# Kernel tuning notes

Measured on AMD Instinct MI355X. Metric: run time of the kernel, lower is better.

Reference implementation:

```python
import jax, jax.numpy as jnp
import numpy as np


def setup_inputs() -> dict:
    key = jax.random.key(0)
    k1, k2, k3 = jax.random.split(key, 3)
    T, D, U = 32768, 1024, 1024
    x = jax.random.normal(k1, (1, T, D), dtype=jnp.float32)
    # scale weights down so gates don't saturate over long sequences
    kernel = jax.random.normal(k2, (D, 4 * U), dtype=jnp.float32) * 0.05
    recurrent_kernel = jax.random.normal(k3, (U, 4 * U), dtype=jnp.float32) * 0.05
    bias = jnp.zeros((4 * U,), dtype=jnp.float32)
    return {"x": x, "kernel": kernel, "recurrent_kernel": recurrent_kernel, "bias": bias}


def reference(x, kernel, recurrent_kernel, bias):
    # x: [1, T, D]; batch is fixed to 1 as in the original layer.
    U = recurrent_kernel.shape[0]
    xt = x[0]                              # [T, D]
    # Input contribution to gates can be precomputed (same math, hoisted out of the loop)
    zx = xt @ kernel + bias                # [T, 4U]

    def step(carry, z_x):
        h, c = carry                       # [U], [U]
        z = z_x + h @ recurrent_kernel     # [4U]
        zi, zf, zg, zo = jnp.split(z, 4)
        i = jax.nn.sigmoid(zi)
        f = jax.nn.sigmoid(zf)
        g = jnp.tanh(zg)
        o = jax.nn.sigmoid(zo)
        c = f * c + i * g
        h = o * jnp.tanh(c)
        return (h, c), h

    h0 = jnp.zeros((U,), dtype=x.dtype)
    c0 = jnp.zeros((U,), dtype=x.dtype)
    _, outputs = jax.lax.scan(step, (h0, c0), zx)   # [T, U]
    return outputs[None, :, :]                      # [1, T, U]
```

## Files before the change

### kernel.cpp

```cpp
#include <hip/hip_runtime.h>
#include <hip/hip_bf16.h>

#define T_STEPS 32768
#define DIM     1024
#define NGATE   4096
#define GWG     128
#define UPW     8

typedef __attribute__((ext_vector_type(8))) short  short8;
typedef __attribute__((ext_vector_type(4))) float  floatx4;

static __device__ __forceinline__ unsigned short f2bf(float f) {
    union { __hip_bfloat16 h; unsigned short u; } cv;
    cv.h = __float2bfloat16(f);
    return cv.u;
}
static __device__ __forceinline__ float fast_sigmoid(float x) {
    float e = __builtin_amdgcn_exp2f(x * -1.442695041f);
    return __builtin_amdgcn_rcpf(1.f + e);
}
static __device__ __forceinline__ float fast_tanh(float x) {
    float e = __builtin_amdgcn_exp2f(x * -2.885390082f);
    return __builtin_amdgcn_rcpf(1.f + e) * 2.f - 1.f;
}


__global__ void conv_x_kernel(const float* __restrict__ x,
                              unsigned short* __restrict__ xb, long n4) {
    long i = (long)blockIdx.x * blockDim.x + threadIdx.x;
    if (i >= n4) return;
    floatx4 v = ((const floatx4*)x)[i];
    unsigned long long p =  (unsigned long long)f2bf(v[0])
                         | ((unsigned long long)f2bf(v[1]) << 16)
                         | ((unsigned long long)f2bf(v[2]) << 32)
                         | ((unsigned long long)f2bf(v[3]) << 48);
    ((unsigned long long*)xb)[i] = p;
}

__global__ void conv_w_kernel(const float* __restrict__ kern,
                              unsigned short* __restrict__ wbt) {
    int idx = blockIdx.x * 256 + threadIdx.x;
    int kb  = idx >> 12;
    int c   = idx & 4095;
    int n = ((c & 1023) >> 3) * 32 + (c >> 10) * 8 + (c & 7);
    unsigned long long p = 0;
#pragma unroll
    for (int i = 0; i < 4; ++i) {
        float f = kern[(size_t)(kb * 4 + i) * NGATE + c];
        p |= (unsigned long long)f2bf(f) << (16 * i);
    }
    ((unsigned long long*)(wbt + (size_t)n * DIM))[kb] = p;
}

__global__ void init_kernel(long long* hbuf8, float* cst) {
    int t = threadIdx.x;
    for (int u = t; u < 1024; u += 256) {
        hbuf8[u]        = ((long long)(-2)) << 32;
        hbuf8[1024 + u] = ((long long)(-1)) << 32;
        cst[u] = 0.f;
    }
}


__global__ __launch_bounds__(256) void gemm_kernel(
        const unsigned short* __restrict__ xb,
        const unsigned short* __restrict__ wbt,
        float* __restrict__ zxf, int t0) {
    __shared__ unsigned short As[64 * 40];
    __shared__ unsigned short Bs[64 * 40];
    const int tid = threadIdx.x;
    const int w = tid >> 6, l = tid & 63;
    const int mBase = t0 + blockIdx.x * 64;
    const int nBase = blockIdx.y * 64;
    const int r  = tid >> 2;
    const int kc = (tid & 3) * 8;
    const int lm = l & 15, kq = l >> 4;

    floatx4 acc[4];
#pragma unroll
    for (int i = 0; i < 4; ++i) acc[i] = (floatx4){0.f, 0.f, 0.f, 0.f};

    for (int kt = 0; kt < DIM; kt += 32) {
        *(uint4*)&As[r * 40 + kc] = *(const uint4*)&xb [(size_t)(mBase + r) * DIM + kt + kc];
        *(uint4*)&Bs[r * 40 + kc] = *(const uint4*)&wbt[(size_t)(nBase + r) * DIM + kt + kc];
        __syncthreads();
        short8 a = *(const short8*)&As[(w * 16 + lm) * 40 + kq * 8];
#pragma unroll
        for (int i = 0; i < 4; ++i) {
            short8 b = *(const short8*)&Bs[(i * 16 + lm) * 40 + kq * 8];
            acc[i] = __builtin_amdgcn_mfma_f32_16x16x32_bf16(a, b, acc[i], 0, 0, 0);
        }
        __syncthreads();
    }
    const int rowq = (l >> 4) * 4;
#pragma unroll
    for (int i = 0; i < 4; ++i)
#pragma unroll
        for (int j = 0; j < 4; ++j) {
            int m = mBase + w * 16 + rowq + j;
            zxf[(size_t)(m - t0) * NGATE + nBase + i * 16 + lm] = acc[i][j];
        }
}


__global__ __launch_bounds__(256, 1) void scan_kernel(
        const float* __restrict__ zxf,
        const float* __restrict__ rker,
        const float* __restrict__ bias,
        float* __restrict__ out,
        long long* hbuf8, float* cst, int t0, int t1) {
    const int wg    = blockIdx.x;
    const int tid   = threadIdx.x;
    const int wave  = tid >> 6, lane = tid & 63;
    const int col32 = lane & 31;
    const int khalf = lane >> 5;
    const int kbase = (wave * 2 + khalf) * 128;
    const int gate  = col32 >> 3, uin = col32 & 7;
    const int c     = gate * 1024 + wg * UPW + uin;

    __shared__ float lds_h[1024];
    __shared__ float lds_part[2][3][32];

    float wr[128];
#pragma unroll
    for (int j = 0; j < 128; ++j)
        wr[j] = rker[(size_t)(kbase + j) * NGATE + c];

    float bias_v = bias[c];
    float cstate = 0.f;
    if (wave == 0 && lane < UPW) cstate = cst[wg * UPW + lane];

    for (int t = t0; t < t1; ++t) {
        const int par  = t & 1;
        const int rpar = (t + 1) & 1;
        const int etag = t - 1;

        float zxv = 0.f;
        if (wave == 0)
            zxv = zxf[(size_t)(t - t0) * NGATE + wg * 32 + col32];

        const long long* hb = hbuf8 + (size_t)rpar * 1024 + wave * 256 + lane * 4;
        int4 p0, p1;
        while (true) {
            asm volatile("global_load_dwordx4 %0, %2, off sc0 sc1\n\t"
                         "global_load_dwordx4 %1, %2, off offset:16 sc0 sc1\n\t"
                         "s_waitcnt vmcnt(0)"
                         : "=v"(p0), "=v"(p1) : "v"(hb) : "memory");
            bool ok = (p0.y == etag) && (p0.w == etag) &&
                      (p1.y == etag) && (p1.w == etag);
            if (__all(ok)) break;
        }

        floatx4 hv4;
        hv4[0] = __int_as_float(p0.x);
        hv4[1] = __int_as_float(p0.z);
        hv4[2] = __int_as_float(p1.x);
        hv4[3] = __int_as_float(p1.z);
        *(floatx4*)&lds_h[wave * 256 + lane * 4] = hv4;

        float z0 = 0.f, z1 = 0.f, z2 = 0.f, z3 = 0.f;
#pragma unroll
        for (int j = 0; j < 32; ++j) {
            floatx4 hv = *(const floatx4*)&lds_h[kbase + j * 4];
            z0 = fmaf(wr[4 * j + 0], hv[0], z0);
            z1 = fmaf(wr[4 * j + 1], hv[1], z1);
            z2 = fmaf(wr[4 * j + 2], hv[2], z2);
            z3 = fmaf(wr[4 * j + 3], hv[3], z3);
        }
        float z = (z0 + z1) + (z2 + z3);
        z += __shfl_down(z, 32);

        if (wave > 0 && lane < 32) lds_part[par][wave - 1][lane] = z;
        __syncthreads();

        if (wave == 0) {
            if (lane < 32) {
                z += lds_part[par][0][lane] + lds_part[par][1][lane] + lds_part[par][2][lane];
                z += bias_v + zxv;
            }
            int u = lane & 7;
            float g0 = __shfl(z,      u);
            float g1 = __shfl(z,  8 + u);
            float g2 = __shfl(z, 16 + u);
            float g3 = __shfl(z, 24 + u);
            if (lane < UPW) {
                float ig = fast_sigmoid(g0);
                float fg = fast_sigmoid(g1);
                float gg = fast_tanh(g2);
                float og = fast_sigmoid(g3);
                cstate = fg * cstate + ig * gg;
                float h = og * fast_tanh(cstate);
                out[(size_t)t * DIM + wg * UPW + lane] = h;
                int2 pr;
                pr.x = __float_as_int(h);
                pr.y = t;
                long long* dst = hbuf8 + (size_t)par * 1024 + wg * UPW + lane;
                asm volatile("global_store_dwordx2 %0, %1, off sc0 sc1"
                             :: "v"(dst), "v"(pr) : "memory");
            }
        }
    }
    if (wave == 0 && lane < UPW) cst[wg * UPW + lane] = cstate;
}


extern "C" void kernel_launch(void* const* d_in, const int* in_sizes, int n_in,
                              void* d_out, int out_size, void* d_ws, size_t ws_size,
                              hipStream_t stream) {
    const float* x    = (const float*)d_in[0];
    const float* kern = (const float*)d_in[1];
    const float* rker = (const float*)d_in[2];
    const float* bias = (const float*)d_in[3];
    float* out = (float*)d_out;

    char* ws = (char*)d_ws;
    size_t off = 0;
    auto alloc = [&](size_t bytes) {
        char* p = ws + off;
        off = (off + bytes + 255) & ~(size_t)255;
        return p;
    };
    unsigned short* wbt = (unsigned short*)alloc((size_t)NGATE * DIM * 2);
    unsigned short* xb  = (unsigned short*)alloc((size_t)T_STEPS * DIM * 2);
    long long* hbuf8 = (long long*)alloc(2 * 1024 * 8);
    float*     cst   = (float*)alloc(1024 * 4);

    size_t avail = ws_size > off ? ws_size - off : 0;
    size_t tcmax = avail / ((size_t)NGATE * 4);
    if (tcmax > T_STEPS) tcmax = T_STEPS;
    int TC = (int)(tcmax & ~(size_t)63);
    if (TC < 64) TC = 64;
    float* zxf = (float*)alloc((size_t)TC * NGATE * 4);

    hipLaunchKernelGGL(conv_w_kernel, dim3(4096), dim3(256), 0, stream, kern, wbt);
    hipLaunchKernelGGL(conv_x_kernel, dim3((T_STEPS * DIM / 4 + 255) / 256), dim3(256),
                       0, stream, x, xb, (long)(T_STEPS * DIM / 4));
    hipLaunchKernelGGL(init_kernel, dim3(1), dim3(256), 0, stream, hbuf8, cst);

    for (int t0 = 0; t0 < T_STEPS; t0 += TC) {
        int tc = (T_STEPS - t0 < TC) ? (T_STEPS - t0) : TC;
        hipLaunchKernelGGL(gemm_kernel, dim3(tc / 64, NGATE / 64), dim3(256),
                           0, stream, xb, wbt, zxf, t0);
        hipLaunchKernelGGL(scan_kernel, dim3(GWG), dim3(256),
                           0, stream, zxf, rker, bias, out, hbuf8, cst, t0, t0 + tc);
    }
}
```

Measured before the change: 68.21 ms.

## Replicate h broadcast buffers and remove intra-block reduction barrier in LSTM scan

Each of the 128 workgroups now polls one of 8 replicated copies of the hidden-state exchange buffer, and each producer writes its h values to all 8 copies, so polling traffic is spread across more memory lines. Work is remapped so each wave owns two units and reduces its dot product with cross-lane shuffles, which removes the LDS partial-sum stage and the wave-0 serial epilogue. The next step's zx value is prefetched. In exchange, each step issues eight times as many global stores, and the poll loop now uses per-element atomic loads instead of two wide loads.

```diff
diff --git a/kernel.cpp b/kernel.cpp
--- a/kernel.cpp
+++ b/kernel.cpp
@@ -6,6 +6,7 @@
 #define NGATE   4096
 #define GWG     128
 #define UPW     8
+#define NREP    8
 
 typedef __attribute__((ext_vector_type(8))) short  short8;
 typedef __attribute__((ext_vector_type(4))) float  floatx4;
@@ -55,8 +56,11 @@
 __global__ void init_kernel(long long* hbuf8, float* cst) {
     int t = threadIdx.x;
     for (int u = t; u < 1024; u += 256) {
-        hbuf8[u]        = ((long long)(-2)) << 32;
-        hbuf8[1024 + u] = ((long long)(-1)) << 32;
+#pragma unroll
+        for (int r = 0; r < NREP; ++r) {
+            hbuf8[(size_t)r * 2048 + u]        = ((long long)(-2)) << 32;
+            hbuf8[(size_t)r * 2048 + 1024 + u] = ((long long)(-1)) << 32;
+        }
         cst[u] = 0.f;
     }
 }
@@ -109,98 +113,104 @@
         const float* __restrict__ bias,
         float* __restrict__ out,
         long long* hbuf8, float* cst, int t0, int t1) {
-    const int wg    = blockIdx.x;
-    const int tid   = threadIdx.x;
-    const int wave  = tid >> 6, lane = tid & 63;
-    const int col32 = lane & 31;
-    const int khalf = lane >> 5;
-    const int kbase = (wave * 2 + khalf) * 128;
-    const int gate  = col32 >> 3, uin = col32 & 7;
-    const int c     = gate * 1024 + wg * UPW + uin;
-
-    __shared__ float lds_h[1024];
-    __shared__ float lds_part[2][3][32];
+    const int wg     = blockIdx.x;
+    const int tid    = threadIdx.x;
+    const int wave   = tid >> 6, lane = tid & 63;
+    const int kslice = lane >> 3;
+    const int idx8   = lane & 7;
+    const int g      = idx8 >> 1;
+    const int du     = idx8 & 1;
+    const int unit   = wg * UPW + 2 * wave + du;
+    const int c      = g * 1024 + unit;
+    const int zxcol  = wg * 32 + g * 8 + 2 * wave + du;
+    const int rep    = wg >> 4;
+
+    __shared__ float lds_h[2][8 * 132];
 
     float wr[128];
 #pragma unroll
     for (int j = 0; j < 128; ++j)
-        wr[j] = rker[(size_t)(kbase + j) * NGATE + c];
+        wr[j] = rker[(size_t)(kslice * 128 + j) * NGATE + c];
 
     float bias_v = bias[c];
     float cstate = 0.f;
-    if (wave == 0 && lane < UPW) cstate = cst[wg * UPW + lane];
+    if (lane < 2) cstate = cst[unit];
+
+    float zx_next = zxf[(size_t)0 * NGATE + zxcol];
+
+    const int stage_idx = (wave * 2 + (lane >> 5)) * 132 + (lane & 31) * 4;
 
     for (int t = t0; t < t1; ++t) {
         const int par  = t & 1;
         const int rpar = (t + 1) & 1;
         const int etag = t - 1;
-
-        float zxv = 0.f;
-        if (wave == 0)
-            zxv = zxf[(size_t)(t - t0) * NGATE + wg * 32 + col32];
-
-        const long long* hb = hbuf8 + (size_t)rpar * 1024 + wave * 256 + lane * 4;
-        int4 p0, p1;
-        while (true) {
-            asm volatile("global_load_dwordx4 %0, %2, off sc0 sc1\n\t"
-                         "global_load_dwordx4 %1, %2, off offset:16 sc0 sc1\n\t"
-                         "s_waitcnt vmcnt(0)"
-                         : "=v"(p0), "=v"(p1) : "v"(hb) : "memory");
-            bool ok = (p0.y == etag) && (p0.w == etag) &&
-                      (p1.y == etag) && (p1.w == etag);
-            if (__all(ok)) break;
-        }
-
-        floatx4 hv4;
-        hv4[0] = __int_as_float(p0.x);
-        hv4[1] = __int_as_float(p0.z);
-        hv4[2] = __int_as_float(p1.x);
-        hv4[3] = __int_as_float(p1.z);
-        *(floatx4*)&lds_h[wave * 256 + lane * 4] = hv4;
+        const float zxv = zx_next;
+
+        const long long* hb = hbuf8 + (size_t)rep * 2048 + (size_t)rpar * 1024
+                              + wave * 256 + lane * 4;
+        bool done = false;
+        do {
+            if (!done) {
+                long long q0 = __hip_atomic_load(hb + 0, __ATOMIC_RELAXED, __HIP_MEMORY_SCOPE_AGENT);
+                long long q1 = __hip_atomic_load(hb + 1, __ATOMIC_RELAXED, __HIP_MEMORY_SCOPE_AGENT);
+                long long q2 = __hip_atomic_load(hb + 2, __ATOMIC_RELAXED, __HIP_MEMORY_SCOPE_AGENT);
+                long long q3 = __hip_atomic_load(hb + 3, __ATOMIC_RELAXED, __HIP_MEMORY_SCOPE_AGENT);
+                if ((int)(q0 >> 32) == etag && (int)(q1 >> 32) == etag &&
+                    (int)(q2 >> 32) == etag && (int)(q3 >> 32) == etag) {
+                    floatx4 hv;
+                    hv[0] = __int_as_float((int)q0);
+                    hv[1] = __int_as_float((int)q1);
+                    hv[2] = __int_as_float((int)q2);
+                    hv[3] = __int_as_float((int)q3);
+                    *(floatx4*)&lds_h[rpar][stage_idx] = hv;
+                    done = true;
+                }
+            }
+        } while (!__all(done));
+        __syncthreads();
 
         float z0 = 0.f, z1 = 0.f, z2 = 0.f, z3 = 0.f;
+        const float* hp = &lds_h[rpar][kslice * 132];
 #pragma unroll
         for (int j = 0; j < 32; ++j) {
-            floatx4 hv = *(const floatx4*)&lds_h[kbase + j * 4];
+            floatx4 hv = *(const floatx4*)&hp[j * 4];
             z0 = fmaf(wr[4 * j + 0], hv[0], z0);
             z1 = fmaf(wr[4 * j + 1], hv[1], z1);
             z2 = fmaf(wr[4 * j + 2], hv[2], z2);
             z3 = fmaf(wr[4 * j + 3], hv[3], z3);
         }
         float z = (z0 + z1) + (z2 + z3);
-        z += __shfl_down(z, 32);
-
-        if (wave > 0 && lane < 32) lds_part[par][wave - 1][lane] = z;
-        __syncthreads();
-
-        if (wave == 0) {
-            if (lane < 32) {
-                z += lds_part[par][0][lane] + lds_part[par][1][lane] + lds_part[par][2][lane];
-                z += bias_v + zxv;
-            }
-            int u = lane & 7;
-            float g0 = __shfl(z,      u);
-            float g1 = __shfl(z,  8 + u);
-            float g2 = __shfl(z, 16 + u);
-            float g3 = __shfl(z, 24 + u);
-            if (lane < UPW) {
-                float ig = fast_sigmoid(g0);
-                float fg = fast_sigmoid(g1);
-                float gg = fast_tanh(g2);
-                float og = fast_sigmoid(g3);
-                cstate = fg * cstate + ig * gg;
-                float h = og * fast_tanh(cstate);
-                out[(size_t)t * DIM + wg * UPW + lane] = h;
-                int2 pr;
-                pr.x = __float_as_int(h);
-                pr.y = t;
-                long long* dst = hbuf8 + (size_t)par * 1024 + wg * UPW + lane;
+        z += __shfl_xor(z, 8);
+        z += __shfl_xor(z, 16);
+        z += __shfl_xor(z, 32);
+        z += bias_v + zxv;
+
+        int dl = lane & 1;
+        float gi = __shfl(z, dl);
+        float gf = __shfl(z, 2 + dl);
+        float gg = __shfl(z, 4 + dl);
+        float go = __shfl(z, 6 + dl);
+        if (lane < 2) {
+            float ig = fast_sigmoid(gi);
+            float fg = fast_sigmoid(gf);
+            float gv = fast_tanh(gg);
+            float og = fast_sigmoid(go);
+            cstate = fg * cstate + ig * gv;
+            float h = og * fast_tanh(cstate);
+            int2 pr;
+            pr.x = __float_as_int(h);
+            pr.y = t;
+            long long* dst = hbuf8 + (size_t)par * 1024 + unit;
+#pragma unroll
+            for (int r = 0; r < NREP; ++r)
                 asm volatile("global_store_dwordx2 %0, %1, off sc0 sc1"
-                             :: "v"(dst), "v"(pr) : "memory");
-            }
-        }
-    }
-    if (wave == 0 && lane < UPW) cst[wg * UPW + lane] = cstate;
+                             :: "v"(dst + (size_t)r * 2048), "v"(pr) : "memory");
+            out[(size_t)t * DIM + unit] = h;
+        }
+        int tn = (t + 1 < t1) ? (t + 1) : t;
+        zx_next = zxf[(size_t)(tn - t0) * NGATE + zxcol];
+    }
+    if (lane < 2) cst[unit] = cstate;
 }
 
 
@@ -222,7 +232,7 @@
     };
     unsigned short* wbt = (unsigned short*)alloc((size_t)NGATE * DIM * 2);
     unsigned short* xb  = (unsigned short*)alloc((size_t)T_STEPS * DIM * 2);
-    long long* hbuf8 = (long long*)alloc(2 * 1024 * 8);
+    long long* hbuf8 = (long long*)alloc((size_t)NREP * 2048 * 8);
     float*     cst   = (float*)alloc(1024 * 4);
 
     size_t avail = ws_size > off ? ws_size - off : 0;
```

After: 103.0 ms. 1.51x slower.
